# Kernel optimization log

Measured on AMD Instinct MI355X. Metric: run time of the kernel, lower is better.

## Reference

```python
import jax, jax.numpy as jnp
import numpy as np

B, S, D = 2, 2048, 1024
KQ_EMB, V_EMB, H = 1024, 1024, 16
KQ_HD, V_HD = KQ_EMB // H, V_EMB // H


def setup_inputs() -> dict:
    key = jax.random.key(0)
    ks = jax.random.split(key, 7)
    scale = 1.0 / np.sqrt(D)
    return {
        "q": jax.random.normal(ks[0], (B, S, D), dtype=jnp.float32),
        "k": jax.random.normal(ks[1], (B, S, D), dtype=jnp.float32),
        "v": jax.random.normal(ks[2], (B, S, D), dtype=jnp.float32),
        "Wq": jax.random.normal(ks[3], (D, KQ_EMB), dtype=jnp.float32) * scale,
        "Wk": jax.random.normal(ks[4], (D, KQ_EMB), dtype=jnp.float32) * scale,
        "Wv": jax.random.normal(ks[5], (D, V_EMB), dtype=jnp.float32) * scale,
        "Wo": jax.random.normal(ks[6], (V_EMB, V_EMB), dtype=jnp.float32) * (1.0 / np.sqrt(V_EMB)),
        "masked": 1,
    }


def reference(q, k, v, Wq, Wk, Wv, Wo, masked):
    Bq, Sq, _ = q.shape
    # projections (Linear, no bias)
    Q = (q @ Wq).reshape(Bq, Sq, H, KQ_HD).transpose(0, 2, 1, 3)  # [B,H,S,hd]
    K = (k @ Wk).reshape(Bq, Sq, H, KQ_HD).transpose(0, 2, 1, 3)
    V = (v @ Wv).reshape(Bq, Sq, H, V_HD).transpose(0, 2, 1, 3)
    scores = jnp.einsum("bhqd,bhkd->bhqk", Q, K) * (1.0 / KQ_HD ** 0.5)
    if masked:
        causal = jnp.tril(jnp.ones((Sq, Sq), dtype=bool))  # True = keep
        scores = jnp.where(causal, scores, jnp.float32(-jnp.inf))
    weights = jax.nn.softmax(scores, axis=-1)
    attn_out = jnp.einsum("bhqk,bhkd->bhqd", weights, V)  # [B,H,S,v_hd]
    merged = attn_out.transpose(0, 2, 1, 3).reshape(Bq, Sq, H * V_HD)
    output = merged @ Wo
    return output, attn_out
```

## Files before the change

### kernel.cpp

```cpp
#include <hip/hip_runtime.h>
#include <math.h>

constexpr int CB = 2, CS = 2048, CD = 1024, CH = 16, CHD = 64;
constexpr int CEMB = 1024;

typedef unsigned short ushort_t;
typedef __attribute__((ext_vector_type(8))) short short8;
typedef __attribute__((ext_vector_type(4))) float f32x4;

__device__ __forceinline__ ushort_t f2bf(float x) {
    unsigned int u = __builtin_bit_cast(unsigned int, x);
    u = u + 0x7fffu + ((u >> 16) & 1u);
    return (ushort_t)(u >> 16);
}
__device__ __forceinline__ float bf2f(ushort_t h) {
    unsigned int u = ((unsigned int)h) << 16;
    return __builtin_bit_cast(float, u);
}

__global__ __launch_bounds__(256) void convert_wt(
    const float* __restrict__ W0, const float* __restrict__ W1,
    const float* __restrict__ W2, const float* __restrict__ W3,
    ushort_t* __restrict__ H0, ushort_t* __restrict__ L0,
    ushort_t* __restrict__ H1, ushort_t* __restrict__ L1,
    ushort_t* __restrict__ H2, ushort_t* __restrict__ L2,
    ushort_t* __restrict__ H3, ushort_t* __restrict__ L3) {
    const float* W;
    ushort_t* Hd;
    ushort_t* Ld;
    switch (blockIdx.z) {
        case 0: W = W0; Hd = H0; Ld = L0; break;
        case 1: W = W1; Hd = H1; Ld = L1; break;
        case 2: W = W2; Hd = H2; Ld = L2; break;
        default: W = W3; Hd = H3; Ld = L3; break;
    }
    const int n0 = blockIdx.x * 64, k0 = blockIdx.y * 64;
    __shared__ float Ls[64][65];
    const int t = threadIdx.x;
#pragma unroll
    for (int rep = 0; rep < 4; rep++) {
        const int r = rep * 16 + (t >> 4);
        const int c4 = (t & 15) * 4;
        *(float4*)&Ls[r][c4] = *(const float4*)&W[(size_t)(k0 + r) * CEMB + n0 + c4];
    }
    __syncthreads();
    const int n = t >> 2, kc = (t & 3) * 16;
#pragma unroll
    for (int c = 0; c < 2; c++) {
        union { ushort_t us[8]; uint4 v; } H, L;
#pragma unroll
        for (int j = 0; j < 8; j++) {
            const float x = Ls[kc + c * 8 + j][n];
            const ushort_t h = f2bf(x);
            H.us[j] = h;
            L.us[j] = f2bf(x - bf2f(h));
        }
        const size_t dst = (size_t)(n0 + n) * CEMB + k0 + kc + c * 8;
        *(uint4*)&Hd[dst] = H.v;
        *(uint4*)&Ld[dst] = L.v;
    }
}

template <bool GATHER_A>
__device__ __forceinline__ void gemm_split_body(
    const float* __restrict__ A, const ushort_t* __restrict__ Bhi,
    const ushort_t* __restrict__ Blo, float* __restrict__ Cf,
    ushort_t* __restrict__ C0, ushort_t* __restrict__ C1, float scale,
    int emode, int M, int N, int K) {
    __shared__ ushort_t As_hi[128 * 32], As_lo[128 * 32];
    __shared__ ushort_t Bs_hi[128 * 32], Bs_lo[128 * 32];
    const int tid = threadIdx.x;
    const int row0 = blockIdx.y * 128, col0 = blockIdx.x * 128;
    const int w = tid >> 6, l = tid & 63, lr = l & 15, lg = l >> 4;
    const int wm = w >> 1, wn = w & 1;

    f32x4 acc[4][4];
#pragma unroll
    for (int i = 0; i < 4; i++)
#pragma unroll
        for (int j = 0; j < 4; j++) acc[i][j] = (f32x4)(0.f);

    const int st_r = tid >> 1;
    const int st_kh = (tid & 1) * 16;

    for (int k0 = 0; k0 < K; k0 += 32) {
        {
            const int gm = row0 + st_r;
            const int gk = k0 + st_kh;
            const float* src;
            if (GATHER_A) {
                const int b_ = gm >> 11, s_ = gm & 2047;
                const int h_ = gk >> 6, d_ = gk & 63;
                src = &A[(((size_t)b_ * CH + h_) * CS + s_) * CHD + d_];
            } else {
                src = &A[(size_t)gm * K + gk];
            }
            float va[16];
#pragma unroll
            for (int r = 0; r < 4; r++)
                *(float4*)&va[r * 4] = *(const float4*)&src[r * 4];
#pragma unroll
            for (int c = 0; c < 2; c++) {
                union { ushort_t us[8]; uint4 v; } H, L;
#pragma unroll
                for (int j = 0; j < 8; j++) {
                    const float x = va[c * 8 + j];
                    const ushort_t h = f2bf(x);
                    H.us[j] = h;
                    L.us[j] = f2bf(x - bf2f(h));
                }
                const int chunk = (st_kh >> 3) + c;
                const int csw = chunk ^ ((st_r >> 1) & 3);
                *(uint4*)&As_hi[st_r * 32 + csw * 8] = H.v;
                *(uint4*)&As_lo[st_r * 32 + csw * 8] = L.v;
            }
        }
        {
            const size_t base = (size_t)(col0 + st_r) * K + k0 + st_kh;
#pragma unroll
            for (int c = 0; c < 2; c++) {
                const uint4 hv = *(const uint4*)&Bhi[base + c * 8];
                const uint4 lv = *(const uint4*)&Blo[base + c * 8];
                const int chunk = (st_kh >> 3) + c;
                const int csw = chunk ^ ((st_r >> 1) & 3);
                *(uint4*)&Bs_hi[st_r * 32 + csw * 8] = hv;
                *(uint4*)&Bs_lo[st_r * 32 + csw * 8] = lv;
            }
        }
        __syncthreads();

        short8 ah[4], al[4], bh[4], bl[4];
#pragma unroll
        for (int i = 0; i < 4; i++) {
            const int r = wm * 64 + i * 16 + lr;
            const int cs = lg ^ ((r >> 1) & 3);
            ah[i] = *(const short8*)&As_hi[r * 32 + cs * 8];
            al[i] = *(const short8*)&As_lo[r * 32 + cs * 8];
        }
#pragma unroll
        for (int j = 0; j < 4; j++) {
            const int cc = wn * 64 + j * 16 + lr;
            const int cs = lg ^ ((cc >> 1) & 3);
            bh[j] = *(const short8*)&Bs_hi[cc * 32 + cs * 8];
            bl[j] = *(const short8*)&Bs_lo[cc * 32 + cs * 8];
        }
#pragma unroll
        for (int j = 0; j < 4; j++)
#pragma unroll
            for (int i = 0; i < 4; i++) {
                acc[i][j] = __builtin_amdgcn_mfma_f32_16x16x32_bf16(
                    al[i], bh[j], acc[i][j], 0, 0, 0);
                acc[i][j] = __builtin_amdgcn_mfma_f32_16x16x32_bf16(
                    ah[i], bl[j], acc[i][j], 0, 0, 0);
                acc[i][j] = __builtin_amdgcn_mfma_f32_16x16x32_bf16(
                    ah[i], bh[j], acc[i][j], 0, 0, 0);
            }
        __syncthreads();
    }

#pragma unroll
    for (int i = 0; i < 4; i++)
#pragma unroll
        for (int j = 0; j < 4; j++) {
            const int cc = col0 + wn * 64 + j * 16 + lr;
#pragma unroll
            for (int r = 0; r < 4; r++) {
                const int cr = row0 + wm * 64 + i * 16 + lg * 4 + r;
                const float vv = acc[i][j][r];
                if (emode == 0) {
                    Cf[(size_t)cr * N + cc] = vv;
                } else {
                    const int b_ = cr >> 11, s_ = cr & 2047;
                    const int h_ = cc >> 6, d_ = cc & 63;
                    if (emode == 1) {
                        const size_t idx =
                            (((size_t)b_ * CH + h_) * CS + s_) * CHD + d_;
                        const float x = vv * scale;
                        const ushort_t hb = f2bf(x);
                        C0[idx] = hb;
                        C1[idx] = f2bf(x - bf2f(hb));
                    } else {
                        C0[(((size_t)b_ * CH + h_) * CHD + d_) * CS + s_] =
                            f2bf(vv);
                    }
                }
            }
        }
}

__global__ __launch_bounds__(256, 2) void qkv_proj(
    const float* __restrict__ q, const float* __restrict__ k,
    const float* __restrict__ v,
    const ushort_t* __restrict__ hq, const ushort_t* __restrict__ lq,
    const ushort_t* __restrict__ hk, const ushort_t* __restrict__ lk,
    const ushort_t* __restrict__ hv, const ushort_t* __restrict__ lv,
    ushort_t* __restrict__ Qhi, ushort_t* __restrict__ Qlo,
    ushort_t* __restrict__ Khi, ushort_t* __restrict__ Klo,
    ushort_t* __restrict__ Vt) {
    const float* A;
    const ushort_t* Bh;
    const ushort_t* Bl;
    ushort_t* C0;
    ushort_t* C1 = nullptr;
    float scale = 1.0f;
    int emode;
    if (blockIdx.z == 0) {
        A = q; Bh = hq; Bl = lq; C0 = Qhi; C1 = Qlo; scale = 0.125f; emode = 1;
    } else if (blockIdx.z == 1) {
        A = k; Bh = hk; Bl = lk; C0 = Khi; C1 = Klo; emode = 1;
    } else {
        A = v; Bh = hv; Bl = lv; C0 = Vt; emode = 2;
    }
    gemm_split_body<false>(A, Bh, Bl, nullptr, C0, C1, scale, emode,
                           CB * CS, CEMB, CD);
}

__global__ __launch_bounds__(256, 2) void out_proj(
    const float* __restrict__ attn, const ushort_t* __restrict__ ho,
    const ushort_t* __restrict__ lo_, float* __restrict__ out) {
    gemm_split_body<true>(attn, ho, lo_, out, nullptr, nullptr, 1.0f, 0,
                          CB * CS, CEMB, CEMB);
}

constexpr int LP = 72;

__global__ __launch_bounds__(256, 2) void flash_mfma(
    const ushort_t* __restrict__ Qhi, const ushort_t* __restrict__ Qlo,
    const ushort_t* __restrict__ Khi, const ushort_t* __restrict__ Klo,
    const ushort_t* __restrict__ Vt, float* __restrict__ O,
    const int* __restrict__ maskedp) {
    __shared__ ushort_t Ks_hi[64 * LP];
    __shared__ ushort_t Ks_lo[64 * LP];
    __shared__ ushort_t Vs[64 * LP];
    __shared__ ushort_t Ps[4][32 * LP];
    const int tid = threadIdx.x;
    const int w = tid >> 6, l = tid & 63, lr = l & 15, lg = l >> 4;
    const int j = blockIdx.x;
    const int bh = blockIdx.y;
    const int masked = maskedp[0];
    const int myqt = (w < 2) ? (31 - j) : j;
    const int q0 = myqt * 64 + (w & 1) * 32;
    const size_t bhoff = (size_t)bh * CS * CHD;

    short8 qh[2][2], ql[2][2];
#pragma unroll
    for (int qf = 0; qf < 2; qf++)
#pragma unroll
        for (int ds = 0; ds < 2; ds++) {
            const size_t off = bhoff + (size_t)(q0 + qf * 16 + lr) * CHD +
                               ds * 32 + lg * 8;
            qh[qf][ds] = *(const short8*)&Qhi[off];
            ql[qf][ds] = *(const short8*)&Qlo[off];
        }

    f32x4 Oacc[2][4];
    float m_i[2][4], l_i[2][4];
#pragma unroll
    for (int qf = 0; qf < 2; qf++)
#pragma unroll
        for (int d = 0; d < 4; d++) Oacc[qf][d] = (f32x4)(0.f);
#pragma unroll
    for (int qf = 0; qf < 2; qf++)
#pragma unroll
        for (int r = 0; r < 4; r++) { m_i[qf][r] = -INFINITY; l_i[qf][r] = 0.f; }

    const int tmax = masked ? (31 - j) : 31;
    const int tBmax = masked ? j : 31;

    const int st_r = tid >> 2;
    const int st_c = (tid & 3);

    for (int t = 0; t <= tmax; t++) {
#pragma unroll
        for (int p = 0; p < 2; p++) {
            const int c = st_c + p * 4;
            const size_t kgl = bhoff + (size_t)(t * 64 + st_r) * CHD + c * 8;
            *(uint4*)&Ks_hi[st_r * LP + c * 8] = *(const uint4*)&Khi[kgl];
            *(uint4*)&Ks_lo[st_r * LP + c * 8] = *(const uint4*)&Klo[kgl];
            const size_t vgl =
                ((size_t)bh * CHD + st_r) * CS + t * 64 + c * 8;
            *(uint4*)&Vs[st_r * LP + c * 8] = *(const uint4*)&Vt[vgl];
        }
        __syncthreads();

        const bool act = (w < 2) || (t <= tBmax);
        if (act) {
            f32x4 S[2][4];
#pragma unroll
            for (int qf = 0; qf < 2; qf++)
#pragma unroll
                for (int kf = 0; kf < 4; kf++) S[qf][kf] = (f32x4)(0.f);
#pragma unroll
            for (int ds = 0; ds < 2; ds++) {
                short8 kh[4], kl[4];
#pragma unroll
                for (int kf = 0; kf < 4; kf++) {
                    const int off = (kf * 16 + lr) * LP + ds * 32 + lg * 8;
                    kh[kf] = *(const short8*)&Ks_hi[off];
                    kl[kf] = *(const short8*)&Ks_lo[off];
                }
#pragma unroll
                for (int qf = 0; qf < 2; qf++)
#pragma unroll
                    for (int kf = 0; kf < 4; kf++) {
                        S[qf][kf] = __builtin_amdgcn_mfma_f32_16x16x32_bf16(
                            ql[qf][ds], kh[kf], S[qf][kf], 0, 0, 0);
                        S[qf][kf] = __builtin_amdgcn_mfma_f32_16x16x32_bf16(
                            qh[qf][ds], kl[kf], S[qf][kf], 0, 0, 0);
                        S[qf][kf] = __builtin_amdgcn_mfma_f32_16x16x32_bf16(
                            qh[qf][ds], kh[kf], S[qf][kf], 0, 0, 0);
                    }
            }

            if (masked && t == myqt) {
#pragma unroll
                for (int qf = 0; qf < 2; qf++)
#pragma unroll
                    for (int kf = 0; kf < 4; kf++)
#pragma unroll
                        for (int r = 0; r < 4; r++) {
                            const int qg = q0 + qf * 16 + lg * 4 + r;
                            const int kg = t * 64 + kf * 16 + lr;
                            if (kg > qg) S[qf][kf][r] = -INFINITY;
                        }
            }

#pragma unroll
            for (int qf = 0; qf < 2; qf++)
#pragma unroll
                for (int r = 0; r < 4; r++) {
                    float mt = fmaxf(fmaxf(S[qf][0][r], S[qf][1][r]),
                                     fmaxf(S[qf][2][r], S[qf][3][r]));
                    mt = fmaxf(mt, __shfl_xor(mt, 1));
                    mt = fmaxf(mt, __shfl_xor(mt, 2));
                    mt = fmaxf(mt, __shfl_xor(mt, 4));
                    mt = fmaxf(mt, __shfl_xor(mt, 8));
                    const float mn = fmaxf(m_i[qf][r], mt);
                    const float corr = __expf(m_i[qf][r] - mn);
                    float rs = 0.f;
#pragma unroll
                    for (int kf = 0; kf < 4; kf++) {
                        const float p = __expf(S[qf][kf][r] - mn);
                        S[qf][kf][r] = p;
                        rs += p;
                    }
                    rs += __shfl_xor(rs, 1);
                    rs += __shfl_xor(rs, 2);
                    rs += __shfl_xor(rs, 4);
                    rs += __shfl_xor(rs, 8);
                    l_i[qf][r] = l_i[qf][r] * corr + rs;
                    m_i[qf][r] = mn;
#pragma unroll
                    for (int df = 0; df < 4; df++) Oacc[qf][df][r] *= corr;
                }

#pragma unroll
            for (int qf = 0; qf < 2; qf++)
#pragma unroll
                for (int kf = 0; kf < 4; kf++)
#pragma unroll
                    for (int r = 0; r < 4; r++) {
                        const float v = S[qf][kf][r];
                        const float vo = __shfl_xor(v, 1);
                        const unsigned int pk =
                            (unsigned int)f2bf(v) |
                            ((unsigned int)f2bf(vo) << 16);
                        if (!(l & 1)) {
                            *(unsigned int*)&Ps[w][(qf * 16 + lg * 4 + r) * LP +
                                                   kf * 16 + lr] = pk;
                        }
                    }

#pragma unroll
            for (int ks = 0; ks < 2; ks++) {
                short8 pa[2], vb[4];
#pragma unroll
                for (int qf = 0; qf < 2; qf++)
                    pa[qf] = *(const short8*)&Ps[w][(qf * 16 + lr) * LP +
                                                    ks * 32 + lg * 8];
#pragma unroll
                for (int df = 0; df < 4; df++)
                    vb[df] = *(const short8*)&Vs[(df * 16 + lr) * LP +
                                                 ks * 32 + lg * 8];
#pragma unroll
                for (int qf = 0; qf < 2; qf++)
#pragma unroll
                    for (int df = 0; df < 4; df++)
                        Oacc[qf][df] = __builtin_amdgcn_mfma_f32_16x16x32_bf16(
                            pa[qf], vb[df], Oacc[qf][df], 0, 0, 0);
            }
        }
        __syncthreads();
    }

#pragma unroll
    for (int qf = 0; qf < 2; qf++)
#pragma unroll
        for (int r = 0; r < 4; r++) {
            const float inv = 1.0f / l_i[qf][r];
            const int qg = q0 + qf * 16 + lg * 4 + r;
#pragma unroll
            for (int df = 0; df < 4; df++) {
                O[bhoff + (size_t)qg * CHD + df * 16 + lr] =
                    Oacc[qf][df][r] * inv;
            }
        }
}

extern "C" void kernel_launch(void* const* d_in, const int* in_sizes, int n_in,
                              void* d_out, int out_size, void* d_ws,
                              size_t ws_size, hipStream_t stream) {
    const float* q  = (const float*)d_in[0];
    const float* k  = (const float*)d_in[1];
    const float* v  = (const float*)d_in[2];
    const float* Wq = (const float*)d_in[3];
    const float* Wk = (const float*)d_in[4];
    const float* Wv = (const float*)d_in[5];
    const float* Wo = (const float*)d_in[6];
    const int* masked = (const int*)d_in[7];

    float* out  = (float*)d_out;
    float* attn = out + (size_t)CB * CS * CEMB;

    const size_t NE = (size_t)CB * CS * CEMB;
    ushort_t* wsb = (ushort_t*)d_ws;
    ushort_t* Qhi = wsb + 0 * NE;
    ushort_t* Qlo = wsb + 1 * NE;
    ushort_t* Khi = wsb + 2 * NE;
    ushort_t* Klo = wsb + 3 * NE;
    ushort_t* Vt  = wsb + 4 * NE;
    ushort_t* wb  = wsb + 5 * NE;
    const size_t WN = (size_t)CEMB * CEMB;
    ushort_t* hq = wb + 0 * WN;  ushort_t* lq = wb + 1 * WN;
    ushort_t* hk = wb + 2 * WN;  ushort_t* lk = wb + 3 * WN;
    ushort_t* hv = wb + 4 * WN;  ushort_t* lv = wb + 5 * WN;
    ushort_t* ho = wb + 6 * WN;  ushort_t* lo_ = wb + 7 * WN;

    const int M = CB * CS;
    dim3 blk(256);

    convert_wt<<<dim3(16, 16, 4), blk, 0, stream>>>(
        Wq, Wk, Wv, Wo, hq, lq, hk, lk, hv, lv, ho, lo_);

    qkv_proj<<<dim3(CEMB / 128, M / 128, 3), blk, 0, stream>>>(
        q, k, v, hq, lq, hk, lk, hv, lv, Qhi, Qlo, Khi, Klo, Vt);

    flash_mfma<<<dim3(16, CB * CH), blk, 0, stream>>>(
        Qhi, Qlo, Khi, Klo, Vt, attn, masked);

    out_proj<<<dim3(CEMB / 128, M / 128), blk, 0, stream>>>(attn, ho, lo_, out);
}
```

Before: 424.0 us.

## Transpose attention MFMA layout and register-prefetch next K/V tile

Swaps the MFMA operand order so each lane holds one query row's scores across keys. Row max and sum reductions then need two cross-lane shuffles instead of four per register, and each query's softmax statistics become a single scalar. P is packed into bf16 pairs without shuffles or lane predication. Separately, the next K/V tile is loaded into registers before the current tile's compute, to hide global load latency at the cost of extra VGPRs.

```diff
diff --git a/kernel.cpp b/kernel.cpp
--- a/kernel.cpp
+++ b/kernel.cpp
@@ -254,15 +254,14 @@
         }
 
     f32x4 Oacc[2][4];
-    float m_i[2][4], l_i[2][4];
-#pragma unroll
-    for (int qf = 0; qf < 2; qf++)
+    float m_i[2], l_i[2];
+#pragma unroll
+    for (int qf = 0; qf < 2; qf++) {
+        m_i[qf] = -INFINITY;
+        l_i[qf] = 0.f;
 #pragma unroll
         for (int d = 0; d < 4; d++) Oacc[qf][d] = (f32x4)(0.f);
-#pragma unroll
-    for (int qf = 0; qf < 2; qf++)
-#pragma unroll
-        for (int r = 0; r < 4; r++) { m_i[qf][r] = -INFINITY; l_i[qf][r] = 0.f; }
+    }
 
     const int tmax = masked ? (31 - j) : 31;
     const int tBmax = masked ? j : 31;
@@ -270,18 +269,40 @@
     const int st_r = tid >> 2;
     const int st_c = (tid & 3);
 
+    uint4 pk_hi[2], pk_lo[2], pv[2];
+#pragma unroll
+    for (int p = 0; p < 2; p++) {
+        const int c = st_c + p * 4;
+        const size_t kgl = bhoff + (size_t)(0 * 64 + st_r) * CHD + c * 8;
+        pk_hi[p] = *(const uint4*)&Khi[kgl];
+        pk_lo[p] = *(const uint4*)&Klo[kgl];
+        const size_t vgl = ((size_t)bh * CHD + st_r) * CS + 0 * 64 + c * 8;
+        pv[p] = *(const uint4*)&Vt[vgl];
+    }
+
     for (int t = 0; t <= tmax; t++) {
 #pragma unroll
         for (int p = 0; p < 2; p++) {
             const int c = st_c + p * 4;
-            const size_t kgl = bhoff + (size_t)(t * 64 + st_r) * CHD + c * 8;
-            *(uint4*)&Ks_hi[st_r * LP + c * 8] = *(const uint4*)&Khi[kgl];
-            *(uint4*)&Ks_lo[st_r * LP + c * 8] = *(const uint4*)&Klo[kgl];
-            const size_t vgl =
-                ((size_t)bh * CHD + st_r) * CS + t * 64 + c * 8;
-            *(uint4*)&Vs[st_r * LP + c * 8] = *(const uint4*)&Vt[vgl];
+            *(uint4*)&Ks_hi[st_r * LP + c * 8] = pk_hi[p];
+            *(uint4*)&Ks_lo[st_r * LP + c * 8] = pk_lo[p];
+            *(uint4*)&Vs[st_r * LP + c * 8] = pv[p];
         }
         __syncthreads();
+
+        if (t < tmax) {
+#pragma unroll
+            for (int p = 0; p < 2; p++) {
+                const int c = st_c + p * 4;
+                const size_t kgl =
+                    bhoff + (size_t)((t + 1) * 64 + st_r) * CHD + c * 8;
+                pk_hi[p] = *(const uint4*)&Khi[kgl];
+                pk_lo[p] = *(const uint4*)&Klo[kgl];
+                const size_t vgl =
+                    ((size_t)bh * CHD + st_r) * CS + (t + 1) * 64 + c * 8;
+                pv[p] = *(const uint4*)&Vt[vgl];
+            }
+        }
 
         const bool act = (w < 2) || (t <= tBmax);
         if (act) {
@@ -304,107 +325,101 @@
 #pragma unroll
                     for (int kf = 0; kf < 4; kf++) {
                         S[qf][kf] = __builtin_amdgcn_mfma_f32_16x16x32_bf16(
-                            ql[qf][ds], kh[kf], S[qf][kf], 0, 0, 0);
+                            kh[kf], ql[qf][ds], S[qf][kf], 0, 0, 0);
                         S[qf][kf] = __builtin_amdgcn_mfma_f32_16x16x32_bf16(
-                            qh[qf][ds], kl[kf], S[qf][kf], 0, 0, 0);
+                            kl[kf], qh[qf][ds], S[qf][kf], 0, 0, 0);
                         S[qf][kf] = __builtin_amdgcn_mfma_f32_16x16x32_bf16(
-                            qh[qf][ds], kh[kf], S[qf][kf], 0, 0, 0);
+                            kh[kf], qh[qf][ds], S[qf][kf], 0, 0, 0);
                     }
             }
 
             if (masked && t == myqt) {
 #pragma unroll
-                for (int qf = 0; qf < 2; qf++)
+                for (int qf = 0; qf < 2; qf++) {
+                    const int qg = q0 + qf * 16 + lr;
 #pragma unroll
                     for (int kf = 0; kf < 4; kf++)
 #pragma unroll
                         for (int r = 0; r < 4; r++) {
-                            const int qg = q0 + qf * 16 + lg * 4 + r;
-                            const int kg = t * 64 + kf * 16 + lr;
+                            const int kg = t * 64 + kf * 16 + 4 * lg + r;
                             if (kg > qg) S[qf][kf][r] = -INFINITY;
                         }
-            }
-
-#pragma unroll
-            for (int qf = 0; qf < 2; qf++)
-#pragma unroll
-                for (int r = 0; r < 4; r++) {
-                    float mt = fmaxf(fmaxf(S[qf][0][r], S[qf][1][r]),
-                                     fmaxf(S[qf][2][r], S[qf][3][r]));
-                    mt = fmaxf(mt, __shfl_xor(mt, 1));
-                    mt = fmaxf(mt, __shfl_xor(mt, 2));
-                    mt = fmaxf(mt, __shfl_xor(mt, 4));
-                    mt = fmaxf(mt, __shfl_xor(mt, 8));
-                    const float mn = fmaxf(m_i[qf][r], mt);
-                    const float corr = __expf(m_i[qf][r] - mn);
-                    float rs = 0.f;
-#pragma unroll
-                    for (int kf = 0; kf < 4; kf++) {
+                }
+            }
+
+#pragma unroll
+            for (int qf = 0; qf < 2; qf++) {
+                float mt = -INFINITY;
+#pragma unroll
+                for (int kf = 0; kf < 4; kf++)
+#pragma unroll
+                    for (int r = 0; r < 4; r++) mt = fmaxf(mt, S[qf][kf][r]);
+                mt = fmaxf(mt, __shfl_xor(mt, 16));
+                mt = fmaxf(mt, __shfl_xor(mt, 32));
+                const float mn = fmaxf(m_i[qf], mt);
+                const float corr = __expf(m_i[qf] - mn);
+                float rs = 0.f;
+#pragma unroll
+                for (int kf = 0; kf < 4; kf++)
+#pragma unroll
+                    for (int r = 0; r < 4; r++) {
                         const float p = __expf(S[qf][kf][r] - mn);
                         S[qf][kf][r] = p;
                         rs += p;
                     }
-                    rs += __shfl_xor(rs, 1);
-                    rs += __shfl_xor(rs, 2);
-                    rs += __shfl_xor(rs, 4);
-                    rs += __shfl_xor(rs, 8);
-                    l_i[qf][r] = l_i[qf][r] * corr + rs;
-                    m_i[qf][r] = mn;
-#pragma unroll
-                    for (int df = 0; df < 4; df++) Oacc[qf][df][r] *= corr;
-                }
-
-#pragma unroll
-            for (int qf = 0; qf < 2; qf++)
+                rs += __shfl_xor(rs, 16);
+                rs += __shfl_xor(rs, 32);
+                l_i[qf] = l_i[qf] * corr + rs;
+                m_i[qf] = mn;
+#pragma unroll
+                for (int df = 0; df < 4; df++) Oacc[qf][df] *= corr;
+
 #pragma unroll
                 for (int kf = 0; kf < 4; kf++)
 #pragma unroll
-                    for (int r = 0; r < 4; r++) {
-                        const float v = S[qf][kf][r];
-                        const float vo = __shfl_xor(v, 1);
+                    for (int r2 = 0; r2 < 2; r2++) {
                         const unsigned int pk =
-                            (unsigned int)f2bf(v) |
-                            ((unsigned int)f2bf(vo) << 16);
-                        if (!(l & 1)) {
-                            *(unsigned int*)&Ps[w][(qf * 16 + lg * 4 + r) * LP +
-                                                   kf * 16 + lr] = pk;
-                        }
+                            (unsigned int)f2bf(S[qf][kf][2 * r2]) |
+                            ((unsigned int)f2bf(S[qf][kf][2 * r2 + 1]) << 16);
+                        *(unsigned int*)&Ps[w][(qf * 16 + lr) * LP + kf * 16 +
+                                               4 * lg + 2 * r2] = pk;
                     }
+            }
 
 #pragma unroll
             for (int ks = 0; ks < 2; ks++) {
-                short8 pa[2], vb[4];
-#pragma unroll
-                for (int qf = 0; qf < 2; qf++)
-                    pa[qf] = *(const short8*)&Ps[w][(qf * 16 + lr) * LP +
-                                                    ks * 32 + lg * 8];
+                short8 vb[4], pb[2];
 #pragma unroll
                 for (int df = 0; df < 4; df++)
                     vb[df] = *(const short8*)&Vs[(df * 16 + lr) * LP +
                                                  ks * 32 + lg * 8];
 #pragma unroll
                 for (int qf = 0; qf < 2; qf++)
+                    pb[qf] = *(const short8*)&Ps[w][(qf * 16 + lr) * LP +
+                                                    ks * 32 + lg * 8];
+#pragma unroll
+                for (int qf = 0; qf < 2; qf++)
 #pragma unroll
                     for (int df = 0; df < 4; df++)
                         Oacc[qf][df] = __builtin_amdgcn_mfma_f32_16x16x32_bf16(
-                            pa[qf], vb[df], Oacc[qf][df], 0, 0, 0);
+                            vb[df], pb[qf], Oacc[qf][df], 0, 0, 0);
             }
         }
         __syncthreads();
     }
 
 #pragma unroll
-    for (int qf = 0; qf < 2; qf++)
-#pragma unroll
-        for (int r = 0; r < 4; r++) {
-            const float inv = 1.0f / l_i[qf][r];
-            const int qg = q0 + qf * 16 + lg * 4 + r;
-#pragma unroll
-            for (int df = 0; df < 4; df++) {
-                O[bhoff + (size_t)qg * CHD + df * 16 + lr] =
+    for (int qf = 0; qf < 2; qf++) {
+        const float inv = 1.0f / l_i[qf];
+        const int qg = q0 + qf * 16 + lr;
+#pragma unroll
+        for (int df = 0; df < 4; df++)
+#pragma unroll
+            for (int r = 0; r < 4; r++) {
+                O[bhoff + (size_t)qg * CHD + df * 16 + 4 * lg + r] =
                     Oacc[qf][df][r] * inv;
             }
-        }
+    }
 }
 
 extern "C" void kernel_launch(void* const* d_in, const int* in_sizes, int n_in,
```

Measured after the change: 378.7 us. 10.7% less time.
